# Kernel tuning notes

Hardware: AMD Instinct MI355X
Metric: run time of the kernel (lower is better)

## Reference

```python
import jax, jax.numpy as jnp
import numpy as np

SIZE = 768
SMALL = SIZE // 4 + 1  # 193
N_ROWS = 16 * 512      # 8192 flattened timesteps
N_CODES = 30000
N_PAIRS = 300000


def setup_inputs() -> dict:
    key = jax.random.key(0)
    ks = jax.random.split(key, 10)
    rnn_output = jax.random.normal(ks[0], (16, 512, SIZE), dtype=jnp.float32)
    weight = jax.random.normal(ks[1], (N_CODES, SIZE + 1), dtype=jnp.float32) * 0.02
    weight1 = jax.random.normal(ks[2], (N_CODES, SMALL), dtype=jnp.float32) * 0.02
    idx0 = jnp.stack([
        jax.random.randint(ks[3], (N_PAIRS,), 0, N_ROWS),
        jax.random.randint(ks[4], (N_PAIRS,), 0, N_CODES),
    ], axis=1).astype(jnp.int64)
    y0 = (jax.random.uniform(ks[5], (N_PAIRS,)) < 0.5).astype(jnp.float32)
    idx1 = jnp.stack([
        jax.random.randint(ks[6], (N_PAIRS,), 0, N_ROWS),
        jax.random.randint(ks[7], (N_PAIRS,), 0, N_CODES),
    ], axis=1).astype(jnp.int64)
    y1 = (jax.random.uniform(ks[8], (N_PAIRS,)) < 0.5).astype(jnp.float32)
    seen0 = jnp.zeros((N_PAIRS,), dtype=jnp.float32)
    seen1 = jnp.zeros((N_PAIRS,), dtype=jnp.float32)
    return {"rnn_output": rnn_output, "weight": weight, "weight1": weight1,
            "idx0": idx0, "y0": y0, "seen0": seen0,
            "idx1": idx1, "y1": y1, "seen1": seen1}


def _embedding_dot(features, table, idx):
    # gather feature rows and code-embedding rows, then row-wise dot -> [N]
    f = features[idx[:, 0]]   # [N, D]
    w = table[idx[:, 1]]      # [N, D]
    return jnp.sum(f * w, axis=-1)


def _bce_logits_sum(logits, targets):
    # stable: log(1 + exp(x)) - x*y, summed
    return jnp.sum(jnp.logaddexp(jnp.float32(0.0), logits) - logits * targets)


def reference(rnn_output, weight, weight1, idx0, y0, seen0, idx1, y1, seen1):
    flat = rnn_output.reshape(-1, SIZE)                     # [B*T, size]
    bias = jnp.ones((flat.shape[0], 1), dtype=flat.dtype)
    rnn_with_bias = jnp.concatenate([flat, bias], axis=1)   # [B*T, size+1]

    final = _embedding_dot(rnn_with_bias, weight, idx0)     # [N]
    loss = _bce_logits_sum(final, y0)

    smaller = rnn_with_bias[:, -SMALL:]                     # [B*T, small]
    final1 = _embedding_dot(smaller, weight1, idx1)         # [N]
    loss1 = _bce_logits_sum(final1, y1)

    return final, loss + loss1
```

## Files before the change

### kernel.cpp

```cpp
#include <hip/hip_runtime.h>
#include <hip/hip_fp16.h>

#define FSIZE   768
#define TW0     769
#define TW1     193
#define COL1    576
#define NPAIRS  300000
#define NCODES  30000
#define NROWS   8192
#define NCB     32768

#define NWAVES0 (NPAIRS / 32)
#define NB0     2344
#define NB1     1176
#define NGRID   (NB0 + NB1)
#define NPART   NGRID

#define PH_B    645
#define PF_B    384
#define PW0_B   1407
#define PW1_B   352
#define NPRE    (PH_B + PF_B + PW0_B + PW1_B)
#define FEAT_U4 393216
#define W0_U4   1440000
#define W1_U4   360000

#define O_FEAT8  ((size_t)0)
#define O_W08    (O_FEAT8 + 1572864)
#define O_W18    (O_W08 + 5760000)
#define O_B0F    (O_W18 + 1440000)
#define O_B1F    (O_B0F + 30000)
#define O_CNT    (O_B1F + 30000)
#define O_CUR    (O_CNT + 65536)
#define O_SREC   (O_CUR + 65536)
#define O_PART   (O_SREC + 2400000)
#define WS_U32   (O_PART + NPART + 64)

#define FSCALE   16.0f
#define WSCALE   64.0f
#define DESCALE  (1.0f / 1024.0f)

typedef float f32x2_t __attribute__((ext_vector_type(2)));

__device__ __forceinline__ float loss_term(float x, float y) {
    float ax = fabsf(x);
    return fmaxf(x, 0.0f) + log1pf(__expf(-ax)) - x * y;
}

__device__ __forceinline__ float4 ld4u(const float* p) {
    float4 v; __builtin_memcpy(&v, p, 16); return v;
}

#if defined(__has_builtin)
# if __has_builtin(__builtin_amdgcn_cvt_pk_f32_fp8)
#  define HW_FP8_DEC 1
# endif
# if __has_builtin(__builtin_amdgcn_cvt_pk_fp8_f32)
#  define HW_FP8_ENC 1
# endif
#endif

__device__ __forceinline__ float sw_fp8_to_f32(unsigned b) {
    unsigned mag = b & 0x7fu;
    unsigned r = ((b & 0x80u) << 24) | ((mag << 20) + 0x3C000000u);
    float f = __uint_as_float(r);
    return mag ? f : 0.0f;
}

template <bool HI>
__device__ __forceinline__ f32x2_t fp8x2_to_f32(unsigned u) {
#ifdef HW_FP8_DEC
    return __builtin_amdgcn_cvt_pk_f32_fp8(u, HI);
#else
    f32x2_t o;
    unsigned lo8 = HI ? ((u >> 16) & 0xffu) : (u & 0xffu);
    unsigned hi8 = HI ? ((u >> 24) & 0xffu) : ((u >> 8) & 0xffu);
    o[0] = sw_fp8_to_f32(lo8);
    o[1] = sw_fp8_to_f32(hi8);
    return o;
#endif
}

__device__ __forceinline__ unsigned sw_f32_to_fp8(float x) {
    unsigned short h = __half_as_ushort(__float2half(x));
    unsigned s = ((unsigned)h >> 8) & 0x80u;
    int e = (h >> 10) & 31;
    unsigned m = h & 1023u;
    if (e >= 23) return s | 0x7eu;
    if (e < 9)  return s;
    unsigned t = ((unsigned)(e - 8) << 3) | (m >> 7);
    unsigned rnd = (m >> 6) & 1u, sticky = (m & 63u) ? 1u : 0u;
    t += (rnd & (sticky | (t & 1u)));
    if (t > 0x7eu) t = 0x7eu;
    return s | t;
}

__device__ __forceinline__ unsigned f32x4_to_fp8(float a, float b, float c, float d) {
#ifdef HW_FP8_ENC
    int u = __builtin_amdgcn_cvt_pk_fp8_f32(a, b, 0, false);
    u = __builtin_amdgcn_cvt_pk_fp8_f32(c, d, u, true);
    return (unsigned)u;
#else
    return sw_f32_to_fp8(a) | (sw_f32_to_fp8(b) << 8)
         | (sw_f32_to_fp8(c) << 16) | (sw_f32_to_fp8(d) << 24);
#endif
}

__device__ __forceinline__ unsigned enc4(float4 v, float sc) {
    return f32x4_to_fp8(v.x * sc, v.y * sc, v.z * sc, v.w * sc);
}

__device__ __forceinline__ float dot16(uint4 u, const float* w, float s) {
    f32x2_t p;
    p = fp8x2_to_f32<false>(u.x); s += p[0] * w[0]  + p[1] * w[1];
    p = fp8x2_to_f32<true >(u.x); s += p[0] * w[2]  + p[1] * w[3];
    p = fp8x2_to_f32<false>(u.y); s += p[0] * w[4]  + p[1] * w[5];
    p = fp8x2_to_f32<true >(u.y); s += p[0] * w[6]  + p[1] * w[7];
    p = fp8x2_to_f32<false>(u.z); s += p[0] * w[8]  + p[1] * w[9];
    p = fp8x2_to_f32<true >(u.z); s += p[0] * w[10] + p[1] * w[11];
    p = fp8x2_to_f32<false>(u.w); s += p[0] * w[12] + p[1] * w[13];
    p = fp8x2_to_f32<true >(u.w); s += p[0] * w[14] + p[1] * w[15];
    return s;
}

__device__ __forceinline__ float dot8(uint2 u, const float* w, float s) {
    f32x2_t p;
    p = fp8x2_to_f32<false>(u.x); s += p[0] * w[0] + p[1] * w[1];
    p = fp8x2_to_f32<true >(u.x); s += p[0] * w[2] + p[1] * w[3];
    p = fp8x2_to_f32<false>(u.y); s += p[0] * w[4] + p[1] * w[5];
    p = fp8x2_to_f32<true >(u.y); s += p[0] * w[6] + p[1] * w[7];
    return s;
}

__device__ __forceinline__ void unpack16(uint4 u, float* w) {
    f32x2_t p;
    p = fp8x2_to_f32<false>(u.x); w[0]  = p[0]; w[1]  = p[1];
    p = fp8x2_to_f32<true >(u.x); w[2]  = p[0]; w[3]  = p[1];
    p = fp8x2_to_f32<false>(u.y); w[4]  = p[0]; w[5]  = p[1];
    p = fp8x2_to_f32<true >(u.y); w[6]  = p[0]; w[7]  = p[1];
    p = fp8x2_to_f32<false>(u.z); w[8]  = p[0]; w[9]  = p[1];
    p = fp8x2_to_f32<true >(u.z); w[10] = p[0]; w[11] = p[1];
    p = fp8x2_to_f32<false>(u.w); w[12] = p[0]; w[13] = p[1];
    p = fp8x2_to_f32<true >(u.w); w[14] = p[0]; w[15] = p[1];
}

__device__ __forceinline__ void unpack8(uint2 u, float* w) {
    f32x2_t p;
    p = fp8x2_to_f32<false>(u.x); w[0] = p[0]; w[1] = p[1];
    p = fp8x2_to_f32<true >(u.x); w[2] = p[0]; w[3] = p[1];
    p = fp8x2_to_f32<false>(u.y); w[4] = p[0]; w[5] = p[1];
    p = fp8x2_to_f32<true >(u.y); w[6] = p[0]; w[7] = p[1];
}

__global__ __launch_bounds__(256) void zero_cnt_kernel(int* __restrict__ cnt) {
    cnt[blockIdx.x * 256 + threadIdx.x] = 0;
}

__global__ __launch_bounds__(256) void fused_pre_kernel(
    const float* __restrict__ feat, const float* __restrict__ w0,
    const float* __restrict__ w1,
    const int* __restrict__ idx0, const int* __restrict__ idx1,
    uint4* __restrict__ feat8, uint4* __restrict__ w08, uint4* __restrict__ w18,
    float* __restrict__ b0f, float* __restrict__ b1f, int* __restrict__ cnt)
{
    const int bid = blockIdx.x;
    if (bid < PH_B) {
        const int t = bid * 256 + threadIdx.x;
        const int NT = PH_B * 256;
#pragma unroll
        for (int k = 0; k < 4; ++k) {
            const int i = t + k * NT;
            if (i < NPAIRS) {
                atomicAdd(&cnt[idx0[2 * i + 1]], 1);
            } else if (i < 2 * NPAIRS) {
                atomicAdd(&cnt[NCB + idx1[2 * (i - NPAIRS) + 1]], 1);
            } else if (i < 2 * NPAIRS + NCODES) {
                const int c = i - 2 * NPAIRS;
                b0f[c] = w0[(size_t)c * TW0 + FSIZE];
            } else if (i < 2 * NPAIRS + 2 * NCODES) {
                const int c = i - 2 * NPAIRS - NCODES;
                b1f[c] = w1[(size_t)c * TW1 + (TW1 - 1)];
            }
        }
    } else if (bid < PH_B + PF_B) {
        const int t = (bid - PH_B) * 256 + threadIdx.x;
        const int NT = PF_B * 256;
        float4 v[16];
#pragma unroll
        for (int k = 0; k < 4; ++k) {
            const float* s = feat + (size_t)(t + k * NT) * 16;
            v[4 * k + 0] = ld4u(s);
            v[4 * k + 1] = ld4u(s + 4);
            v[4 * k + 2] = ld4u(s + 8);
            v[4 * k + 3] = ld4u(s + 12);
        }
#pragma unroll
        for (int k = 0; k < 4; ++k) {
            uint4 o;
            o.x = enc4(v[4 * k + 0], FSCALE);
            o.y = enc4(v[4 * k + 1], FSCALE);
            o.z = enc4(v[4 * k + 2], FSCALE);
            o.w = enc4(v[4 * k + 3], FSCALE);
            feat8[t + k * NT] = o;
        }
    } else if (bid < PH_B + PF_B + PW0_B) {
        const int t = (bid - PH_B - PF_B) * 256 + threadIdx.x;
        const int NT = PW0_B * 256;
        float4 v[16];
#pragma unroll
        for (int k = 0; k < 4; ++k) {
            int i = t + k * NT;
            if (i >= W0_U4) i = W0_U4 - 1;
            const int c = i / 48;
            const int e = (i - c * 48) * 16;
            const float* s = w0 + (size_t)c * TW0 + e;
            v[4 * k + 0] = ld4u(s);
            v[4 * k + 1] = ld4u(s + 4);
            v[4 * k + 2] = ld4u(s + 8);
            v[4 * k + 3] = ld4u(s + 12);
        }
#pragma unroll
        for (int k = 0; k < 4; ++k) {
            const int i = t + k * NT;
            if (i < W0_U4) {
                uint4 o;
                o.x = enc4(v[4 * k + 0], WSCALE);
                o.y = enc4(v[4 * k + 1], WSCALE);
                o.z = enc4(v[4 * k + 2], WSCALE);
                o.w = enc4(v[4 * k + 3], WSCALE);
                w08[i] = o;
            }
        }
    } else {
        const int t = (bid - PH_B - PF_B - PW0_B) * 256 + threadIdx.x;
        const int NT = PW1_B * 256;
        float4 v[16];
#pragma unroll
        for (int k = 0; k < 4; ++k) {
            int i = t + k * NT;
            if (i >= W1_U4) i = W1_U4 - 1;
            const int c = i / 12;
            const int e = (i - c * 12) * 16;
            const float* s = w1 + (size_t)c * TW1 + e;
            v[4 * k + 0] = ld4u(s);
            v[4 * k + 1] = ld4u(s + 4);
            v[4 * k + 2] = ld4u(s + 8);
            v[4 * k + 3] = ld4u(s + 12);
        }
#pragma unroll
        for (int k = 0; k < 4; ++k) {
            const int i = t + k * NT;
            if (i < W1_U4) {
                uint4 o;
                o.x = enc4(v[4 * k + 0], WSCALE);
                o.y = enc4(v[4 * k + 1], WSCALE);
                o.z = enc4(v[4 * k + 2], WSCALE);
                o.w = enc4(v[4 * k + 3], WSCALE);
                w18[i] = o;
            }
        }
    }
}

__global__ __launch_bounds__(1024) void scan2_kernel(const int* __restrict__ cnt,
                                                     int* __restrict__ cursor) {
    __shared__ int wsum[16];
    __shared__ int wbase[16];
    const int t = threadIdx.x;
    const int lane = t & 63, wv = t >> 6;
    const int4* c4 = (const int4*)cnt + (size_t)t * 16;
    int4 v[16];
#pragma unroll
    for (int j = 0; j < 16; ++j) v[j] = c4[j];
    int s = 0;
#pragma unroll
    for (int j = 0; j < 16; ++j) {
        int a;
        a = v[j].x; v[j].x = s; s += a;
        a = v[j].y; v[j].y = s; s += a;
        a = v[j].z; v[j].z = s; s += a;
        a = v[j].w; v[j].w = s; s += a;
    }
    int incl = s;
#pragma unroll
    for (int off = 1; off < 64; off <<= 1) {
        int u = __shfl_up(incl, off, 64);
        if (lane >= off) incl += u;
    }
    if (lane == 63) wsum[wv] = incl;
    __syncthreads();
    if (wv == 0 && lane < 16) {
        int mysum = wsum[lane];
        int winc = mysum;
#pragma unroll
        for (int off = 1; off < 16; off <<= 1) {
            int u = __shfl_up(winc, off, 64);
            if (lane >= off) winc += u;
        }
        wbase[lane] = winc - mysum;
    }
    __syncthreads();
    const int base = wbase[wv] + incl - s;
    int4* cu = (int4*)cursor + (size_t)t * 16;
#pragma unroll
    for (int j = 0; j < 16; ++j)
        cu[j] = make_int4(base + v[j].x, base + v[j].y, base + v[j].z, base + v[j].w);
}

__global__ __launch_bounds__(256) void scatter2_kernel(
    const int* __restrict__ idx0, const float* __restrict__ y0,
    const int* __restrict__ idx1, const float* __restrict__ y1,
    int* __restrict__ cursor, uint4* __restrict__ srec, float* __restrict__ loss_out)
{
    const int tid = blockIdx.x * 256 + threadIdx.x;
    if (tid == 0) loss_out[0] = 0.0f;
#pragma unroll
    for (int k = 0; k < 2; ++k) {
        const int t = tid + k * 300032;
        if (t < NPAIRS) {
            int r = idx0[2 * t], c = idx0[2 * t + 1];
            int pos = atomicAdd(&cursor[c], 1);
            srec[pos] = make_uint4((unsigned)r, (unsigned)c, __float_as_uint(y0[t]), (unsigned)t);
        } else if (t < 2 * NPAIRS) {
            int p = t - NPAIRS;
            int r = idx1[2 * p], c = idx1[2 * p + 1];
            int pos = atomicAdd(&cursor[NCB + c], 1);
            srec[pos] = make_uint4((unsigned)r, (unsigned)c, __float_as_uint(y1[p]), (unsigned)p);
        }
    }
}

__global__ __launch_bounds__(256) void main3_kernel(
    const unsigned char* __restrict__ feat8, const unsigned char* __restrict__ w08,
    const unsigned char* __restrict__ w18,
    const float* __restrict__ b0f, const float* __restrict__ b1f,
    const uint4* __restrict__ srec,
    float* __restrict__ out_final, float* __restrict__ loss_out)
{
    __shared__ float bsum[4];
    const int lane = threadIdx.x & 63;
    const int wv   = threadIdx.x >> 6;
    float wavesum = 0.f;

    if (blockIdx.x < NB0) {
        const int work = (blockIdx.x & 7) * (NB0 / 8) + (blockIdx.x >> 3);
        const int wid = work * 4 + wv;
        if (wid < NWAVES0) {
            const int g = lane >> 4, sub = lane & 15;
            const uint4 rec = srec[(size_t)wid * 32 + 8 * g + (sub & 7)];
            int prev_c = -1;
            float wc[48];
            float wb = 0.f, lg = 0.f;
#pragma unroll
            for (int j = 0; j < 8; ++j) {
                const int src = (lane & 48) | j;
                const int r = __shfl((int)rec.x, src, 64);
                const int c = __shfl((int)rec.y, src, 64);
                if (c != prev_c) {
                    prev_c = c;
                    const unsigned char* wr = w08 + (size_t)c * FSIZE + 48 * sub;
                    uint4 wu0 = *(const uint4*)wr;
                    uint4 wu1 = *(const uint4*)(wr + 16);
                    uint4 wu2 = *(const uint4*)(wr + 32);
                    unpack16(wu0, &wc[0]);
                    unpack16(wu1, &wc[16]);
                    unpack16(wu2, &wc[32]);
                    wb = b0f[c];
                }
                const unsigned char* fr = feat8 + (size_t)r * FSIZE + 48 * sub;
                uint4 f0 = *(const uint4*)fr;
                uint4 f1 = *(const uint4*)(fr + 16);
                uint4 f2 = *(const uint4*)(fr + 32);
                float s = dot16(f0, &wc[0], 0.f);
                s = dot16(f1, &wc[16], s);
                s = dot16(f2, &wc[32], s);
                s += __shfl_xor(s, 8, 64);
                s += __shfl_xor(s, 4, 64);
                s += __shfl_xor(s, 2, 64);
                s += __shfl_xor(s, 1, 64);
                lg = (sub == j) ? s * DESCALE + wb : lg;
            }
            float ll = 0.f;
            if (sub < 8) {
                out_final[rec.w] = lg;
                ll = loss_term(lg, __uint_as_float(rec.z));
            }
#pragma unroll
            for (int m = 32; m; m >>= 1) ll += __shfl_xor(ll, m, 64);
            wavesum = ll;
        }
    } else {
        const int tb = blockIdx.x - NB0;
        const int work1 = (tb & 7) * (NB1 / 8) + (tb >> 3);
        const long base = (long)(work1 * 4 + wv) * 64;
        if (base < NPAIRS) {
            const int g = lane >> 3, sub = lane & 7;
            long lpos = base + 8 * g + sub;
            if (lpos > NPAIRS - 1) lpos = NPAIRS - 1;
            const uint4 rec = srec[(size_t)NPAIRS + lpos];
            int prev_c = -1;
            float wc[24];
            float wb = 0.f, lg = 0.f;
#pragma unroll
            for (int j = 0; j < 8; ++j) {
                const bool valid = (base + 8 * g + j) < NPAIRS;
                const int src = (lane & 56) | j;
                const int r = __shfl((int)rec.x, src, 64);
                const int c = __shfl((int)rec.y, src, 64);
                if (valid) {
                    if (c != prev_c) {
                        prev_c = c;
                        const unsigned char* wr = w18 + (size_t)c * 192 + 24 * sub;
                        uint2 wu0 = *(const uint2*)wr;
                        uint2 wu1 = *(const uint2*)(wr + 8);
                        uint2 wu2 = *(const uint2*)(wr + 16);
                        unpack8(wu0, &wc[0]);
                        unpack8(wu1, &wc[8]);
                        unpack8(wu2, &wc[16]);
                        wb = b1f[c];
                    }
                    const unsigned char* fr = feat8 + (size_t)r * FSIZE + COL1 + 24 * sub;
                    uint2 f0 = *(const uint2*)fr;
                    uint2 f1 = *(const uint2*)(fr + 8);
                    uint2 f2 = *(const uint2*)(fr + 16);
                    float s = dot8(f0, &wc[0], 0.f);
                    s = dot8(f1, &wc[8], s);
                    s = dot8(f2, &wc[16], s);
                    s += __shfl_xor(s, 4, 64);
                    s += __shfl_xor(s, 2, 64);
                    s += __shfl_xor(s, 1, 64);
                    lg = (sub == j) ? s * DESCALE + wb : lg;
                }
            }
            float ll = 0.f;
            if ((base + 8 * g + sub) < NPAIRS)
                ll = loss_term(lg, __uint_as_float(rec.z));
#pragma unroll
            for (int m = 32; m; m >>= 1) ll += __shfl_xor(ll, m, 64);
            wavesum = ll;
        }
    }

    if (lane == 0) bsum[wv] = wavesum;
    __syncthreads();
    if (threadIdx.x == 0) {
        float t = bsum[0] + bsum[1] + bsum[2] + bsum[3];
        atomicAdd(loss_out, t);
    }
}

__global__ __launch_bounds__(1024) void reduce_kernel(
    const float* __restrict__ partial, int n, float* __restrict__ out)
{
    __shared__ float sh[1024];
    float s = 0.0f;
    for (int i = threadIdx.x; i < n; i += 1024) s += partial[i];
    sh[threadIdx.x] = s;
    __syncthreads();
    for (int off = 512; off; off >>= 1) {
        if ((int)threadIdx.x < off) sh[threadIdx.x] += sh[threadIdx.x + off];
        __syncthreads();
    }
    if (threadIdx.x == 0) out[0] = sh[0];
}

__global__ __launch_bounds__(256) void task0_kernel(
    const float* __restrict__ feat, const float* __restrict__ wt,
    const int* __restrict__ idx, const float* __restrict__ y,
    float* __restrict__ out_final, float* __restrict__ partial)
{
    __shared__ float lsum[4];
    const int lane = threadIdx.x & 63;
    const int wv = threadIdx.x >> 6;
    const int pair = blockIdx.x * 4 + wv;
    const int r = idx[2 * pair];
    const int c = idx[2 * pair + 1];
    const float4* f4 = (const float4*)(feat + (size_t)r * FSIZE);
    const float* wrow = wt + (size_t)c * TW0;
    float s = 0.0f;
#pragma unroll
    for (int k = 0; k < 3; ++k) {
        const int j = lane + (k << 6);
        float4 f = f4[j];
        float4 w = ld4u(wrow + 4 * j);
        s += f.x * w.x + f.y * w.y + f.z * w.z + f.w * w.w;
    }
#pragma unroll
    for (int m = 32; m; m >>= 1) s += __shfl_xor(s, m, 64);
    if (lane == 0) {
        const float logit = s + wrow[FSIZE];
        out_final[pair] = logit;
        lsum[wv] = loss_term(logit, y[pair]);
    }
    __syncthreads();
    if (threadIdx.x == 0)
        partial[blockIdx.x] = lsum[0] + lsum[1] + lsum[2] + lsum[3];
}

__global__ __launch_bounds__(256) void task1_kernel(
    const float* __restrict__ feat, const float* __restrict__ wt,
    const int* __restrict__ idx, const float* __restrict__ y,
    float* __restrict__ partial)
{
    __shared__ float lsum[16];
    const int lane = threadIdx.x & 63;
    const int wv = threadIdx.x >> 6;
    const int sub = lane & 15;
    const int pg = lane >> 4;
    const int pair = (blockIdx.x * 4 + wv) * 4 + pg;
    const int r = idx[2 * pair];
    const int c = idx[2 * pair + 1];
    const float4* f4 = (const float4*)(feat + (size_t)r * FSIZE + COL1);
    const float* wrow = wt + (size_t)c * TW1;
    float s = 0.0f;
#pragma unroll
    for (int k = 0; k < 3; ++k) {
        const int j = sub + (k << 4);
        float4 f = f4[j];
        float4 w = ld4u(wrow + 4 * j);
        s += f.x * w.x + f.y * w.y + f.z * w.z + f.w * w.w;
    }
#pragma unroll
    for (int m = 8; m; m >>= 1) s += __shfl_xor(s, m, 64);
    if (sub == 0) {
        const float logit = s + wrow[TW1 - 1];
        lsum[wv * 4 + pg] = loss_term(logit, y[pair]);
    }
    __syncthreads();
    if (threadIdx.x == 0) {
        float t = 0.0f;
#pragma unroll
        for (int i = 0; i < 16; ++i) t += lsum[i];
        partial[blockIdx.x] = t;
    }
}

extern "C" void kernel_launch(void* const* d_in, const int* in_sizes, int n_in,
                              void* d_out, int out_size, void* d_ws, size_t ws_size,
                              hipStream_t stream) {
    const float* feat = (const float*)d_in[0];
    const float* w0   = (const float*)d_in[1];
    const float* w1   = (const float*)d_in[2];
    const int*   idx0 = (const int*)d_in[3];
    const float* y0   = (const float*)d_in[4];
    const int*   idx1 = (const int*)d_in[6];
    const float* y1   = (const float*)d_in[7];

    float* out = (float*)d_out;
    unsigned* ws = (unsigned*)d_ws;

    if (ws_size >= WS_U32 * 4) {
        unsigned char* feat8 = (unsigned char*)(ws + O_FEAT8);
        unsigned char* w08   = (unsigned char*)(ws + O_W08);
        unsigned char* w18   = (unsigned char*)(ws + O_W18);
        float* b0f   = (float*)(ws + O_B0F);
        float* b1f   = (float*)(ws + O_B1F);
        int*   cnt   = (int*)(ws + O_CNT);
        int*   cursor= (int*)(ws + O_CUR);
        uint4* srec  = (uint4*)(ws + O_SREC);

        zero_cnt_kernel<<<256, 256, 0, stream>>>(cnt);
        fused_pre_kernel<<<NPRE, 256, 0, stream>>>(
            feat, w0, w1, idx0, idx1,
            (uint4*)feat8, (uint4*)w08, (uint4*)w18, b0f, b1f, cnt);
        scan2_kernel<<<1, 1024, 0, stream>>>(cnt, cursor);
        scatter2_kernel<<<1172, 256, 0, stream>>>(
            idx0, y0, idx1, y1, cursor, srec, out + NPAIRS);
        main3_kernel<<<NGRID, 256, 0, stream>>>(
            feat8, w08, w18, b0f, b1f, srec, out, out + NPAIRS);
    } else {
        float* part = (float*)ws;
        const int nb0 = NPAIRS / 4;
        const int nb1 = NPAIRS / 16;
        task0_kernel<<<nb0, 256, 0, stream>>>(feat, w0, idx0, y0, out, part);
        task1_kernel<<<nb1, 256, 0, stream>>>(feat, w1, idx1, y1, part + nb0);
        reduce_kernel<<<1, 1024, 0, stream>>>(part, nb0 + nb1, out + NPAIRS);
    }
}
```

Measured before the change: 174.0 us.

## Split code-count histogram and scatter cursors into eight replicas to cut atomic contention

Replaces the single global per-code counter array with eight replicated histograms, indexed by block id modulo eight, for both the counting and the scatter cursor atomics. Adds a reduction kernel to total the replicas, reuses the scan on those totals, and adds a kernel that derives a per-replica starting cursor. The histogram and scatter blocks are widened to one element per thread. The aim is to spread atomic traffic on popular codes across more addresses and channels, at the cost of two extra kernel launches and more workspace memory traffic.

```diff
diff --git a/kernel.cpp b/kernel.cpp
--- a/kernel.cpp
+++ b/kernel.cpp
@@ -16,7 +16,7 @@
 #define NGRID   (NB0 + NB1)
 #define NPART   NGRID
 
-#define PH_B    645
+#define PH_B    2580
 #define PF_B    384
 #define PW0_B   1407
 #define PW1_B   352
@@ -24,17 +24,19 @@
 #define FEAT_U4 393216
 #define W0_U4   1440000
 #define W1_U4   360000
+#define NSC     2344
 
 #define O_FEAT8  ((size_t)0)
 #define O_W08    (O_FEAT8 + 1572864)
 #define O_W18    (O_W08 + 5760000)
 #define O_B0F    (O_W18 + 1440000)
 #define O_B1F    (O_B0F + 30000)
-#define O_CNT    (O_B1F + 30000)
-#define O_CUR    (O_CNT + 65536)
-#define O_SREC   (O_CUR + 65536)
-#define O_PART   (O_SREC + 2400000)
-#define WS_U32   (O_PART + NPART + 64)
+#define O_HIST   (O_B1F + 30000)
+#define O_TOT    (O_HIST + 524288)
+#define O_BASE   (O_TOT + 65536)
+#define O_CUR    (O_BASE + 65536)
+#define O_SREC   (O_CUR + 524288)
+#define WS_U32   (O_SREC + 2400000 + 64)
 
 #define FSCALE   16.0f
 #define WSCALE   64.0f
@@ -152,8 +154,8 @@
     p = fp8x2_to_f32<true >(u.y); w[6] = p[0]; w[7] = p[1];
 }
 
-__global__ __launch_bounds__(256) void zero_cnt_kernel(int* __restrict__ cnt) {
-    cnt[blockIdx.x * 256 + threadIdx.x] = 0;
+__global__ __launch_bounds__(256) void zero8_kernel(int4* __restrict__ h4) {
+    h4[blockIdx.x * 256 + threadIdx.x] = make_int4(0, 0, 0, 0);
 }
 
 __global__ __launch_bounds__(256) void fused_pre_kernel(
@@ -161,26 +163,22 @@
     const float* __restrict__ w1,
     const int* __restrict__ idx0, const int* __restrict__ idx1,
     uint4* __restrict__ feat8, uint4* __restrict__ w08, uint4* __restrict__ w18,
-    float* __restrict__ b0f, float* __restrict__ b1f, int* __restrict__ cnt)
+    float* __restrict__ b0f, float* __restrict__ b1f, int* __restrict__ hist)
 {
     const int bid = blockIdx.x;
     if (bid < PH_B) {
-        const int t = bid * 256 + threadIdx.x;
-        const int NT = PH_B * 256;
-#pragma unroll
-        for (int k = 0; k < 4; ++k) {
-            const int i = t + k * NT;
-            if (i < NPAIRS) {
-                atomicAdd(&cnt[idx0[2 * i + 1]], 1);
-            } else if (i < 2 * NPAIRS) {
-                atomicAdd(&cnt[NCB + idx1[2 * (i - NPAIRS) + 1]], 1);
-            } else if (i < 2 * NPAIRS + NCODES) {
-                const int c = i - 2 * NPAIRS;
-                b0f[c] = w0[(size_t)c * TW0 + FSIZE];
-            } else if (i < 2 * NPAIRS + 2 * NCODES) {
-                const int c = i - 2 * NPAIRS - NCODES;
-                b1f[c] = w1[(size_t)c * TW1 + (TW1 - 1)];
-            }
+        const int i = bid * 256 + threadIdx.x;
+        int* h = hist + (size_t)(bid & 7) * 65536;
+        if (i < NPAIRS) {
+            atomicAdd(&h[idx0[2 * i + 1]], 1);
+        } else if (i < 2 * NPAIRS) {
+            atomicAdd(&h[NCB + idx1[2 * (i - NPAIRS) + 1]], 1);
+        } else if (i < 2 * NPAIRS + NCODES) {
+            const int c = i - 2 * NPAIRS;
+            b0f[c] = w0[(size_t)c * TW0 + FSIZE];
+        } else if (i < 2 * NPAIRS + 2 * NCODES) {
+            const int c = i - 2 * NPAIRS - NCODES;
+            b1f[c] = w1[(size_t)c * TW1 + (TW1 - 1)];
         }
     } else if (bid < PH_B + PF_B) {
         const int t = (bid - PH_B) * 256 + threadIdx.x;
@@ -262,6 +260,15 @@
     }
 }
 
+__global__ __launch_bounds__(256) void sumx_kernel(const int* __restrict__ hist,
+                                                   int* __restrict__ tot) {
+    const int c = blockIdx.x * 256 + threadIdx.x;
+    int s = 0;
+#pragma unroll
+    for (int x = 0; x < 8; ++x) s += hist[(size_t)x * 65536 + c];
+    tot[c] = s;
+}
+
 __global__ __launch_bounds__(1024) void scan2_kernel(const int* __restrict__ cnt,
                                                      int* __restrict__ cursor) {
     __shared__ int wsum[16];
@@ -307,26 +314,35 @@
         cu[j] = make_int4(base + v[j].x, base + v[j].y, base + v[j].z, base + v[j].w);
 }
 
-__global__ __launch_bounds__(256) void scatter2_kernel(
+__global__ __launch_bounds__(256) void cursor8_kernel(
+    const int* __restrict__ hist, const int* __restrict__ base,
+    int* __restrict__ cur) {
+    const int c = blockIdx.x * 256 + threadIdx.x;
+    int run = base[c];
+#pragma unroll
+    for (int x = 0; x < 8; ++x) {
+        cur[(size_t)x * 65536 + c] = run;
+        run += hist[(size_t)x * 65536 + c];
+    }
+}
+
+__global__ __launch_bounds__(256) void scatter8_kernel(
     const int* __restrict__ idx0, const float* __restrict__ y0,
     const int* __restrict__ idx1, const float* __restrict__ y1,
-    int* __restrict__ cursor, uint4* __restrict__ srec, float* __restrict__ loss_out)
+    int* __restrict__ cur, uint4* __restrict__ srec, float* __restrict__ loss_out)
 {
-    const int tid = blockIdx.x * 256 + threadIdx.x;
-    if (tid == 0) loss_out[0] = 0.0f;
-#pragma unroll
-    for (int k = 0; k < 2; ++k) {
-        const int t = tid + k * 300032;
-        if (t < NPAIRS) {
-            int r = idx0[2 * t], c = idx0[2 * t + 1];
-            int pos = atomicAdd(&cursor[c], 1);
-            srec[pos] = make_uint4((unsigned)r, (unsigned)c, __float_as_uint(y0[t]), (unsigned)t);
-        } else if (t < 2 * NPAIRS) {
-            int p = t - NPAIRS;
-            int r = idx1[2 * p], c = idx1[2 * p + 1];
-            int pos = atomicAdd(&cursor[NCB + c], 1);
-            srec[pos] = make_uint4((unsigned)r, (unsigned)c, __float_as_uint(y1[p]), (unsigned)p);
-        }
+    const int t = blockIdx.x * 256 + threadIdx.x;
+    int* mycur = cur + (size_t)(blockIdx.x & 7) * 65536;
+    if (t == 0) loss_out[0] = 0.0f;
+    if (t < NPAIRS) {
+        int r = idx0[2 * t], c = idx0[2 * t + 1];
+        int pos = atomicAdd(&mycur[c], 1);
+        srec[pos] = make_uint4((unsigned)r, (unsigned)c, __float_as_uint(y0[t]), (unsigned)t);
+    } else if (t < 2 * NPAIRS) {
+        int p = t - NPAIRS;
+        int r = idx1[2 * p], c = idx1[2 * p + 1];
+        int pos = atomicAdd(&mycur[NCB + c], 1);
+        srec[pos] = make_uint4((unsigned)r, (unsigned)c, __float_as_uint(y1[p]), (unsigned)p);
     }
 }
 
@@ -555,17 +571,21 @@
         unsigned char* w18   = (unsigned char*)(ws + O_W18);
         float* b0f   = (float*)(ws + O_B0F);
         float* b1f   = (float*)(ws + O_B1F);
-        int*   cnt   = (int*)(ws + O_CNT);
-        int*   cursor= (int*)(ws + O_CUR);
+        int*   hist  = (int*)(ws + O_HIST);
+        int*   tot   = (int*)(ws + O_TOT);
+        int*   base  = (int*)(ws + O_BASE);
+        int*   cur   = (int*)(ws + O_CUR);
         uint4* srec  = (uint4*)(ws + O_SREC);
 
-        zero_cnt_kernel<<<256, 256, 0, stream>>>(cnt);
+        zero8_kernel<<<512, 256, 0, stream>>>((int4*)hist);
         fused_pre_kernel<<<NPRE, 256, 0, stream>>>(
             feat, w0, w1, idx0, idx1,
-            (uint4*)feat8, (uint4*)w08, (uint4*)w18, b0f, b1f, cnt);
-        scan2_kernel<<<1, 1024, 0, stream>>>(cnt, cursor);
-        scatter2_kernel<<<1172, 256, 0, stream>>>(
-            idx0, y0, idx1, y1, cursor, srec, out + NPAIRS);
+            (uint4*)feat8, (uint4*)w08, (uint4*)w18, b0f, b1f, hist);
+        sumx_kernel<<<256, 256, 0, stream>>>(hist, tot);
+        scan2_kernel<<<1, 1024, 0, stream>>>(tot, base);
+        cursor8_kernel<<<256, 256, 0, stream>>>(hist, base, cur);
+        scatter8_kernel<<<NSC, 256, 0, stream>>>(
+            idx0, y0, idx1, y1, cur, srec, out + NPAIRS);
         main3_kernel<<<NGRID, 256, 0, stream>>>(
             feat8, w08, w18, b0f, b1f, srec, out, out + NPAIRS);
     } else {
```

Result: no change. 177.1 us (+1.8%).
